# Kernel tuning notes

Measured on AMD Instinct MI355X. Metric: run time of the kernel, lower is better.

Reference implementation:

```python
import jax, jax.numpy as jnp
import numpy as np

B, V, NV, NR, N, E, D, H, OUT, L = 4, 20, 8000, 200, 8000, 200000, 128, 128, 64, 3
DECAY = 0.03


def setup_inputs() -> dict:
    key = jax.random.key(0)
    ks = jax.random.split(key, 16)
    node_ids = jax.random.randint(ks[0], (N,), 0, NV)
    rel_ids = jax.random.randint(ks[1], (E,), 0, NR)
    edge_index = jax.random.randint(ks[2], (2, E), 0, N)
    batch = jnp.repeat(jnp.arange(B), N // B)  # sorted graph assignment, 2000 nodes/graph
    visit_node = (jax.random.uniform(ks[3], (B, V, NV)) < 0.3).astype(jnp.float32)
    ehr_nodes = (jax.random.uniform(ks[4], (B, NV)) < 0.1).astype(jnp.float32)
    s = lambda k, shape: jax.random.normal(k, shape, jnp.float32) * 0.05
    return dict(
        node_ids=node_ids, rel_ids=rel_ids, edge_index=edge_index, batch=batch,
        visit_node=visit_node, ehr_nodes=ehr_nodes,
        node_emb_w=s(ks[5], (NV, D)), rel_emb_w=s(ks[6], (NR, D)),
        lin_w=s(ks[7], (D, H)), lin_b=jnp.zeros((H,), jnp.float32),
        alpha_w=s(ks[8], (L, H)), alpha_b=jnp.zeros((L,), jnp.float32),
        beta_w=s(ks[9], (L, NV)), beta_b=jnp.zeros((L,), jnp.float32),
        conv_w=s(ks[10], (L, H, H)), conv_b=jnp.zeros((L, H), jnp.float32),
        wr_w=s(ks[11], (L, H)), wr_b=jnp.zeros((L,), jnp.float32),
        mlp_w=s(ks[12], (2 * H, OUT)), mlp_b=jnp.zeros((OUT,), jnp.float32),
    )


def reference(node_ids, rel_ids, edge_index, batch, visit_node, ehr_nodes,
              node_emb_w, rel_emb_w, lin_w, lin_b, alpha_w, alpha_b,
              beta_w, beta_b, conv_w, conv_b, wr_w, wr_b, mlp_w, mlp_b):
    # shared input projection (torch: self.lin applied to node and edge embeddings)
    x = node_emb_w[node_ids] @ lin_w + lin_b          # [N,H]
    edge_attr = rel_emb_w[rel_ids] @ lin_w + lin_b    # [E,H]

    # pack per-graph node features into dense [B, NV, H] (x_new in torch, fixed across layers)
    counts = jax.ops.segment_sum(jnp.ones((N,), jnp.float32), batch, B)            # [B]
    starts = jnp.concatenate([jnp.zeros((1,), jnp.int32),
                              jnp.cumsum(counts.astype(jnp.int32))[:-1]])
    local = jnp.arange(N) - starts[batch]                                          # position within graph
    x_pad = jnp.zeros((B, NV, H), jnp.float32).at[batch, local].set(x)

    lam = jnp.exp(DECAY * (V - jnp.arange(V, dtype=jnp.float32)))[None, :, None]   # [1,V,1]
    src, dst = edge_index[0], edge_index[1]
    eb, en = batch[src], node_ids[src]

    for l in range(L):
        # alpha attention over visits (softmax on visit axis)
        feat = visit_node[..., None] * x_pad[:, None]                              # [B,V,NV,H]
        alpha = jax.nn.softmax(jnp.einsum('bvnh,h->bvn', feat, alpha_w[l]) + alpha_b[l], axis=1)
        # beta: time-decayed visit attention
        beta = jnp.tanh(visit_node @ beta_w[l] + beta_b[l])[:, :, None] * lam      # [B,V,1]
        attn_full = alpha * beta                                                   # [B,V,NV]
        attn_e = attn_full[eb, 0, en][:, None]                                     # [E,1] (visit idx 0 as in source)
        # BiAttentionGNNConv: gather-mul-relu-scatter with edge attention
        w_rel = (edge_attr @ wr_w[l] + wr_b[l])[:, None]                           # [E,1]
        msg = jax.nn.relu(x[src] * attn_e + w_rel * edge_attr)                     # [E,H]
        agg = jax.ops.segment_sum(msg, dst, N)                                     # scatter-add to targets
        x = jax.nn.relu((agg + x) @ conv_w[l] + conv_b[l])                         # eps=0 -> (1+eps)*x = x; dropout=eval

    # joint patient representation
    x_graph = jax.ops.segment_sum(x, batch, B) / counts[:, None]                   # global mean pool
    x_node = (ehr_nodes @ node_emb_w) / jnp.sum(ehr_nodes, axis=1, keepdims=True)  # [B,D]
    x_node = x_node @ lin_w + lin_b
    logits = jnp.concatenate([x_graph, x_node], axis=1) @ mlp_w + mlp_b            # [B,OUT]
    return logits
```

## Files before the change

kernel.cpp:

```cpp
#include <hip/hip_runtime.h>

#define NN  8000
#define EE  200000
#define BB  4
#define VV  20
#define NVV 8000
#define NRR 200
#define HH  128
#define OO  64
#define LL  3
#define NPB 8
#define NG  2000

__global__ __launch_bounds__(128) void k_proj_nodes(
    const int* __restrict__ node_ids, const float* __restrict__ emb,
    const float* __restrict__ lin_w, const float* __restrict__ lin_b,
    const float* __restrict__ alpha_w, float* __restrict__ x,
    float* __restrict__ snode)
{
  int blk = blockIdx.x, t = threadIdx.x;
  __shared__ float er[NPB][HH];
  __shared__ float part[LL][NPB][2];
  int base = blk * NPB;
  #pragma unroll
  for (int n = 0; n < NPB; ++n)
    er[n][t] = emb[node_ids[base + n] * HH + t];
  __syncthreads();
  float bt = lin_b[t];
  float acc[NPB];
  #pragma unroll
  for (int n = 0; n < NPB; ++n) acc[n] = bt;
  for (int d4 = 0; d4 < HH / 4; ++d4) {
    float e4[NPB][4];
    #pragma unroll
    for (int n = 0; n < NPB; ++n) {
      float4 v = *(const float4*)&er[n][d4 * 4];
      e4[n][0] = v.x; e4[n][1] = v.y; e4[n][2] = v.z; e4[n][3] = v.w;
    }
    #pragma unroll
    for (int j = 0; j < 4; ++j) {
      float lwv = lin_w[(d4 * 4 + j) * HH + t];
      #pragma unroll
      for (int n = 0; n < NPB; ++n) acc[n] += e4[n][j] * lwv;
    }
  }
  #pragma unroll
  for (int n = 0; n < NPB; ++n) x[(base + n) * HH + t] = acc[n];
  #pragma unroll
  for (int l = 0; l < LL; ++l) {
    float aw = alpha_w[l * HH + t];
    #pragma unroll
    for (int n = 0; n < NPB; ++n) {
      float v = acc[n] * aw;
      for (int off = 32; off > 0; off >>= 1) v += __shfl_down(v, off, 64);
      if ((t & 63) == 0) part[l][n][t >> 6] = v;
    }
  }
  __syncthreads();
  if (t < LL * NPB) {
    int l = t / NPB, n = t % NPB;
    snode[l * NN + base + n] = part[l][n][0] + part[l][n][1];
  }
}

__global__ __launch_bounds__(128) void k_prb(
    const float* __restrict__ rel_emb, const float* __restrict__ lin_w,
    const float* __restrict__ lin_b, const float* __restrict__ wr_w,
    const float* __restrict__ wr_b, const float* __restrict__ visit_node,
    const float* __restrict__ beta_w, const float* __restrict__ beta_b,
    float* __restrict__ wrelp, float* __restrict__ beta0,
    int* __restrict__ iz, float* __restrict__ fz)
{
  int blk = blockIdx.x, t = threadIdx.x;
  int idx = blk * 128 + t;
  if (idx < 2 * NN) iz[idx] = 0;
  if (idx < BB * HH * 2 + BB) fz[idx] = 0.f;
  if (blk < NRR) {
    __shared__ float row[HH];
    __shared__ float part[LL][2];
    row[t] = rel_emb[blk * HH + t];
    __syncthreads();
    float acc = lin_b[t];
    #pragma unroll 4
    for (int d = 0; d < HH; ++d) acc += row[d] * lin_w[d * HH + t];
    #pragma unroll
    for (int l = 0; l < LL; ++l) {
      float v = acc * wr_w[l * HH + t];
      for (int off = 32; off > 0; off >>= 1) v += __shfl_down(v, off, 64);
      if ((t & 63) == 0) part[l][t >> 6] = v;
    }
    __syncthreads();
    #pragma unroll
    for (int l = 0; l < LL; ++l) {
      float rd = part[l][0] + part[l][1] + wr_b[l];
      wrelp[(l * NRR + blk) * HH + t] = rd * acc;
    }
  } else {
    int j = blk - NRR;
    int l = j >> 2, b = j & 3;
    float acc = 0.f;
    for (int n = t; n < NVV; n += 128)
      acc += visit_node[(b * VV + 0) * NVV + n] * beta_w[l * NVV + n];
    for (int off = 32; off > 0; off >>= 1) acc += __shfl_down(acc, off, 64);
    __shared__ float bred[2];
    if ((t & 63) == 0) bred[t >> 6] = acc;
    __syncthreads();
    if (t == 0)
      beta0[l * BB + b] = tanhf(bred[0] + bred[1] + beta_b[l]) * expf(0.03f * 20.0f);
  }
}

__global__ __launch_bounds__(256) void k_anode_hist(
    const int* __restrict__ node_ids, const int* __restrict__ batch,
    const int* __restrict__ edge_index, const float* __restrict__ visit_node,
    const float* __restrict__ snode, const float* __restrict__ alpha_b,
    const float* __restrict__ beta0, float* __restrict__ anode,
    int* __restrict__ deg)
{
  int idx = blockIdx.x * 256 + threadIdx.x;
  if (idx < EE) atomicAdd(&deg[edge_index[EE + idx]], 1);
  if (idx >= NN) return;
  int b = batch[idx], nid = node_ids[idx];
  float vn[VV];
  #pragma unroll
  for (int v = 0; v < VV; ++v) vn[v] = visit_node[(b * VV + v) * NVV + nid];
  #pragma unroll
  for (int l = 0; l < LL; ++l) {
    float s = (nid < NG) ? snode[l * NN + b * NG + nid] : 0.0f;
    float ab = alpha_b[l];
    float m = -1e30f;
    #pragma unroll
    for (int v = 0; v < VV; ++v) m = fmaxf(m, vn[v] * s + ab);
    float sum = 0.f;
    #pragma unroll
    for (int v = 0; v < VV; ++v) sum += expf(vn[v] * s + ab - m);
    anode[l * NN + idx] = (expf(vn[0] * s + ab - m) / sum) * beta0[l * BB + b];
  }
}

__global__ __launch_bounds__(1024) void k_scan(const int* __restrict__ deg,
                                               int* __restrict__ row_ptr)
{
  int t = threadIdx.x;
  __shared__ int ps[1024];
  int local[8];
  int base = t * 8;
  int s = 0;
  #pragma unroll
  for (int j = 0; j < 8; ++j) {
    int idx = base + j;
    int v = (idx < NN) ? deg[idx] : 0;
    local[j] = s; s += v;
  }
  ps[t] = s;
  __syncthreads();
  for (int off = 1; off < 1024; off <<= 1) {
    int v = (t >= off) ? ps[t - off] : 0;
    __syncthreads();
    ps[t] += v;
    __syncthreads();
  }
  int excl = (t == 0) ? 0 : ps[t - 1];
  #pragma unroll
  for (int j = 0; j < 8; ++j) {
    int idx = base + j;
    if (idx < NN) row_ptr[idx] = excl + local[j];
  }
  if (t == 1023) row_ptr[NN] = ps[1023];
}

__global__ void k_scatter(const int* __restrict__ edge_index, const int* __restrict__ rel_ids,
                          const int* __restrict__ row_ptr, int* __restrict__ cursor,
                          int2* __restrict__ csr_sr)
{
  int e = blockIdx.x * 256 + threadIdx.x;
  if (e >= EE) return;
  int dst = edge_index[EE + e];
  int p = row_ptr[dst] + atomicAdd(&cursor[dst], 1);
  csr_sr[p] = make_int2(edge_index[e], rel_ids[e]);
}

__global__ __launch_bounds__(256) void k_gather_conv(
    const int* __restrict__ row_ptr, const int2* __restrict__ csr_sr,
    const float* __restrict__ anode, const float* __restrict__ xin,
    const float* __restrict__ wrelp, const float* __restrict__ conv_w,
    const float* __restrict__ conv_b, float* __restrict__ xout, int l)
{
  int t = threadIdx.x;
  int sub = t >> 5, lane = t & 31;
  int i = blockIdx.x * NPB + sub;
  __shared__ float aggrow[NPB][HH];
  const float4* __restrict__ xin4 = (const float4*)xin;
  const float4* __restrict__ wr4 = (const float4*)wrelp + (size_t)l * NRR * 32;
  const float4* __restrict__ cw4 = (const float4*)conv_w + (size_t)l * HH * 32;
  const float* __restrict__ an = anode + (size_t)l * NN;

  float4 acc = xin4[i * 32 + lane];
  int k0 = row_ptr[i], k1 = row_ptr[i + 1];
  int k = k0;
  for (; k + 3 < k1; k += 4) {
    int2 s0 = csr_sr[k],     s1 = csr_sr[k + 1];
    int2 s2 = csr_sr[k + 2], s3 = csr_sr[k + 3];
    float a0 = an[s0.x], a1 = an[s1.x], a2 = an[s2.x], a3 = an[s3.x];
    float4 x0 = xin4[s0.x * 32 + lane], w0 = wr4[s0.y * 32 + lane];
    float4 x1 = xin4[s1.x * 32 + lane], w1 = wr4[s1.y * 32 + lane];
    float4 x2 = xin4[s2.x * 32 + lane], w2 = wr4[s2.y * 32 + lane];
    float4 x3 = xin4[s3.x * 32 + lane], w3 = wr4[s3.y * 32 + lane];
    acc.x += fmaxf(x0.x * a0 + w0.x, 0.f) + fmaxf(x1.x * a1 + w1.x, 0.f)
           + fmaxf(x2.x * a2 + w2.x, 0.f) + fmaxf(x3.x * a3 + w3.x, 0.f);
    acc.y += fmaxf(x0.y * a0 + w0.y, 0.f) + fmaxf(x1.y * a1 + w1.y, 0.f)
           + fmaxf(x2.y * a2 + w2.y, 0.f) + fmaxf(x3.y * a3 + w3.y, 0.f);
    acc.z += fmaxf(x0.z * a0 + w0.z, 0.f) + fmaxf(x1.z * a1 + w1.z, 0.f)
           + fmaxf(x2.z * a2 + w2.z, 0.f) + fmaxf(x3.z * a3 + w3.z, 0.f);
    acc.w += fmaxf(x0.w * a0 + w0.w, 0.f) + fmaxf(x1.w * a1 + w1.w, 0.f)
           + fmaxf(x2.w * a2 + w2.w, 0.f) + fmaxf(x3.w * a3 + w3.w, 0.f);
  }
  for (; k < k1; ++k) {
    int2 s0 = csr_sr[k];
    float a0 = an[s0.x];
    float4 x0 = xin4[s0.x * 32 + lane], w0 = wr4[s0.y * 32 + lane];
    acc.x += fmaxf(x0.x * a0 + w0.x, 0.f);
    acc.y += fmaxf(x0.y * a0 + w0.y, 0.f);
    acc.z += fmaxf(x0.z * a0 + w0.z, 0.f);
    acc.w += fmaxf(x0.w * a0 + w0.w, 0.f);
  }
  *(float4*)&aggrow[sub][lane * 4] = acc;
  __syncthreads();

  float4 o = ((const float4*)conv_b)[l * 32 + lane];
  for (int d4 = 0; d4 < HH / 4; ++d4) {
    float4 ag = *(const float4*)&aggrow[sub][d4 * 4];
    float4 c0 = cw4[(d4 * 4 + 0) * 32 + lane];
    float4 c1 = cw4[(d4 * 4 + 1) * 32 + lane];
    float4 c2 = cw4[(d4 * 4 + 2) * 32 + lane];
    float4 c3 = cw4[(d4 * 4 + 3) * 32 + lane];
    o.x += ag.x * c0.x + ag.y * c1.x + ag.z * c2.x + ag.w * c3.x;
    o.y += ag.x * c0.y + ag.y * c1.y + ag.z * c2.y + ag.w * c3.y;
    o.z += ag.x * c0.z + ag.y * c1.z + ag.z * c2.z + ag.w * c3.z;
    o.w += ag.x * c0.w + ag.y * c1.w + ag.z * c2.w + ag.w * c3.w;
  }
  o.x = fmaxf(o.x, 0.f); o.y = fmaxf(o.y, 0.f);
  o.z = fmaxf(o.z, 0.f); o.w = fmaxf(o.w, 0.f);
  ((float4*)xout)[i * 32 + lane] = o;
}

__global__ __launch_bounds__(128) void k_pool(
    const float* __restrict__ x, const float* __restrict__ ehr,
    const float* __restrict__ emb, float* __restrict__ xg_raw,
    float* __restrict__ xn_raw, float* __restrict__ denom)
{
  int t = threadIdx.x;
  if (blockIdx.x < 64) {
    int b = blockIdx.x >> 4, c = blockIdx.x & 15;
    const int per = NG / 16;
    int base = b * NG + c * per;
    float acc = 0.f;
    for (int i = 0; i < per; ++i) acc += x[(base + i) * HH + t];
    atomicAdd(&xg_raw[b * HH + t], acc);
  } else {
    int ib = blockIdx.x - 64;
    int b = ib >> 5, c = ib & 31;
    const int per = NVV / 32;
    int base = c * per;
    float acc = 0.f;
    for (int n = base; n < base + per; ++n)
      acc += ehr[b * NVV + n] * emb[n * HH + t];
    atomicAdd(&xn_raw[b * HH + t], acc);
    __shared__ float red[128];
    float dsum = 0.f;
    for (int n = base + t; n < base + per; n += 128) dsum += ehr[b * NVV + n];
    red[t] = dsum;
    __syncthreads();
    for (int s = 64; s > 0; s >>= 1) {
      if (t < s) red[t] += red[t + s];
      __syncthreads();
    }
    if (t == 0) atomicAdd(&denom[b], red[0]);
  }
}

__global__ __launch_bounds__(128) void k_final(
    const float* __restrict__ xg_raw, const float* __restrict__ xn_raw,
    const float* __restrict__ denom, const float* __restrict__ lin_w,
    const float* __restrict__ lin_b, const float* __restrict__ mlp_w,
    const float* __restrict__ mlp_b, float* __restrict__ out)
{
  int b = blockIdx.x, t = threadIdx.x;
  __shared__ float xg[HH], xn[HH], xnp[HH];
  xg[t] = xg_raw[b * HH + t] * (1.0f / NG);
  xn[t] = xn_raw[b * HH + t] / denom[b];
  __syncthreads();
  float a3 = lin_b[t];
  #pragma unroll 4
  for (int d = 0; d < HH; ++d) a3 += xn[d] * lin_w[d * HH + t];
  xnp[t] = a3;
  __syncthreads();
  if (t < OO) {
    float a4 = mlp_b[t];
    #pragma unroll 4
    for (int h = 0; h < HH; ++h)
      a4 += xg[h] * mlp_w[h * OO + t] + xnp[h] * mlp_w[(HH + h) * OO + t];
    out[b * OO + t] = a4;
  }
}

extern "C" void kernel_launch(void* const* d_in, const int* in_sizes, int n_in,
                              void* d_out, int out_size, void* d_ws, size_t ws_size,
                              hipStream_t stream) {
  const int*   node_ids   = (const int*)d_in[0];
  const int*   rel_ids    = (const int*)d_in[1];
  const int*   edge_index = (const int*)d_in[2];
  const int*   batch      = (const int*)d_in[3];
  const float* visit_node = (const float*)d_in[4];
  const float* ehr        = (const float*)d_in[5];
  const float* node_emb   = (const float*)d_in[6];
  const float* rel_emb    = (const float*)d_in[7];
  const float* lin_w      = (const float*)d_in[8];
  const float* lin_b      = (const float*)d_in[9];
  const float* alpha_w    = (const float*)d_in[10];
  const float* alpha_b    = (const float*)d_in[11];
  const float* beta_w     = (const float*)d_in[12];
  const float* beta_b     = (const float*)d_in[13];
  const float* conv_w     = (const float*)d_in[14];
  const float* conv_b     = (const float*)d_in[15];
  const float* wr_w       = (const float*)d_in[16];
  const float* wr_b       = (const float*)d_in[17];
  const float* mlp_w      = (const float*)d_in[18];
  const float* mlp_b      = (const float*)d_in[19];
  float* out = (float*)d_out;

  float* ws = (float*)d_ws;
  float* xA     = ws; ws += NN * HH;
  float* xB     = ws; ws += NN * HH;
  float* wrelp  = ws; ws += LL * NRR * HH;
  float* snode  = ws; ws += LL * NN;
  float* beta0  = ws; ws += LL * BB;
  float* anode  = ws; ws += LL * NN;
  float* xg_raw = ws; ws += BB * HH;
  float* xn_raw = ws; ws += BB * HH;
  float* denom  = ws; ws += BB;
  int* iws      = (int*)ws;
  int* deg      = iws; iws += NN;
  int* cursor   = iws; iws += NN;
  int* row_ptr  = iws; iws += NN + 2;
  int2* csr_sr  = (int2*)iws;

  hipLaunchKernelGGL(k_proj_nodes, dim3(NN / NPB), dim3(HH), 0, stream,
                     node_ids, node_emb, lin_w, lin_b, alpha_w, xA, snode);
  hipLaunchKernelGGL(k_prb, dim3(NRR + LL * BB), dim3(HH), 0, stream,
                     rel_emb, lin_w, lin_b, wr_w, wr_b, visit_node, beta_w,
                     beta_b, wrelp, beta0, deg, xg_raw);
  hipLaunchKernelGGL(k_anode_hist, dim3((EE + 255) / 256), dim3(256), 0, stream,
                     node_ids, batch, edge_index, visit_node, snode, alpha_b,
                     beta0, anode, deg);
  hipLaunchKernelGGL(k_scan, dim3(1), dim3(1024), 0, stream, deg, row_ptr);
  hipLaunchKernelGGL(k_scatter, dim3((EE + 255) / 256), dim3(256), 0, stream,
                     edge_index, rel_ids, row_ptr, cursor, csr_sr);
  const float* xin = xA;
  float* xout = xB;
  for (int l = 0; l < LL; ++l) {
    hipLaunchKernelGGL(k_gather_conv, dim3(NN / NPB), dim3(256), 0, stream,
                       row_ptr, csr_sr, anode, xin, wrelp, conv_w, conv_b, xout, l);
    const float* tmp = xin; xin = xout; xout = (float*)tmp;
  }
  hipLaunchKernelGGL(k_pool, dim3(64 + 128), dim3(HH), 0, stream,
                     xB, ehr, node_emb, xg_raw, xn_raw, denom);
  hipLaunchKernelGGL(k_final, dim3(BB), dim3(HH), 0, stream,
                     xg_raw, xn_raw, denom, lin_w, lin_b, mlp_w, mlp_b, out);
}
```

Measured before the change: 311.3 us.

## Split each node's edge gather across two half-warps and halve nodes per block

Each node's incoming-edge list is now split between two 32-lane groups, and the partial sums are combined through shared memory. This halves the serial gather chain per node and doubles the number of blocks to raise memory-level parallelism. The dense conv matmul is redistributed so 64 lanes each produce a float2 of output. In exchange it adds extra shared-memory traffic and synchronisation, and the conv-weight loads are now amortised over 4 nodes per block instead of 8.

```diff
diff --git a/kernel.cpp b/kernel.cpp
--- a/kernel.cpp
+++ b/kernel.cpp
@@ -10,6 +10,7 @@
 #define OO  64
 #define LL  3
 #define NPB 8
+#define NPG 4
 #define NG  2000
 
 __global__ __launch_bounds__(128) void k_proj_nodes(
@@ -187,18 +188,27 @@
     const float* __restrict__ conv_b, float* __restrict__ xout, int l)
 {
   int t = threadIdx.x;
-  int sub = t >> 5, lane = t & 31;
-  int i = blockIdx.x * NPB + sub;
-  __shared__ float aggrow[NPB][HH];
+  int node_sub = t >> 6;
+  int half = (t >> 5) & 1;
+  int lane = t & 31;
+  int lane64 = t & 63;
+  int i = blockIdx.x * NPG + node_sub;
+  __shared__ float part[2][NPG][HH];
   const float4* __restrict__ xin4 = (const float4*)xin;
+  const float2* __restrict__ xin2 = (const float2*)xin;
   const float4* __restrict__ wr4 = (const float4*)wrelp + (size_t)l * NRR * 32;
-  const float4* __restrict__ cw4 = (const float4*)conv_w + (size_t)l * HH * 32;
   const float* __restrict__ an = anode + (size_t)l * NN;
 
-  float4 acc = xin4[i * 32 + lane];
   int k0 = row_ptr[i], k1 = row_ptr[i + 1];
-  int k = k0;
-  for (; k + 3 < k1; k += 4) {
+  int cnt = k1 - k0;
+  int halfcnt = (cnt + 1) >> 1;
+  int ks = k0 + half * halfcnt;
+  int ke = half ? k1 : (k0 + halfcnt);
+
+  float4 accA = make_float4(0.f, 0.f, 0.f, 0.f);
+  float4 accB = make_float4(0.f, 0.f, 0.f, 0.f);
+  int k = ks;
+  for (; k + 3 < ke; k += 4) {
     int2 s0 = csr_sr[k],     s1 = csr_sr[k + 1];
     int2 s2 = csr_sr[k + 2], s3 = csr_sr[k + 3];
     float a0 = an[s0.x], a1 = an[s1.x], a2 = an[s2.x], a3 = an[s3.x];
@@ -206,42 +216,52 @@
     float4 x1 = xin4[s1.x * 32 + lane], w1 = wr4[s1.y * 32 + lane];
     float4 x2 = xin4[s2.x * 32 + lane], w2 = wr4[s2.y * 32 + lane];
     float4 x3 = xin4[s3.x * 32 + lane], w3 = wr4[s3.y * 32 + lane];
-    acc.x += fmaxf(x0.x * a0 + w0.x, 0.f) + fmaxf(x1.x * a1 + w1.x, 0.f)
-           + fmaxf(x2.x * a2 + w2.x, 0.f) + fmaxf(x3.x * a3 + w3.x, 0.f);
-    acc.y += fmaxf(x0.y * a0 + w0.y, 0.f) + fmaxf(x1.y * a1 + w1.y, 0.f)
-           + fmaxf(x2.y * a2 + w2.y, 0.f) + fmaxf(x3.y * a3 + w3.y, 0.f);
-    acc.z += fmaxf(x0.z * a0 + w0.z, 0.f) + fmaxf(x1.z * a1 + w1.z, 0.f)
-           + fmaxf(x2.z * a2 + w2.z, 0.f) + fmaxf(x3.z * a3 + w3.z, 0.f);
-    acc.w += fmaxf(x0.w * a0 + w0.w, 0.f) + fmaxf(x1.w * a1 + w1.w, 0.f)
-           + fmaxf(x2.w * a2 + w2.w, 0.f) + fmaxf(x3.w * a3 + w3.w, 0.f);
-  }
-  for (; k < k1; ++k) {
+    accA.x += fmaxf(x0.x * a0 + w0.x, 0.f) + fmaxf(x1.x * a1 + w1.x, 0.f);
+    accA.y += fmaxf(x0.y * a0 + w0.y, 0.f) + fmaxf(x1.y * a1 + w1.y, 0.f);
+    accA.z += fmaxf(x0.z * a0 + w0.z, 0.f) + fmaxf(x1.z * a1 + w1.z, 0.f);
+    accA.w += fmaxf(x0.w * a0 + w0.w, 0.f) + fmaxf(x1.w * a1 + w1.w, 0.f);
+    accB.x += fmaxf(x2.x * a2 + w2.x, 0.f) + fmaxf(x3.x * a3 + w3.x, 0.f);
+    accB.y += fmaxf(x2.y * a2 + w2.y, 0.f) + fmaxf(x3.y * a3 + w3.y, 0.f);
+    accB.z += fmaxf(x2.z * a2 + w2.z, 0.f) + fmaxf(x3.z * a3 + w3.z, 0.f);
+    accB.w += fmaxf(x2.w * a2 + w2.w, 0.f) + fmaxf(x3.w * a3 + w3.w, 0.f);
+  }
+  for (; k < ke; ++k) {
     int2 s0 = csr_sr[k];
     float a0 = an[s0.x];
     float4 x0 = xin4[s0.x * 32 + lane], w0 = wr4[s0.y * 32 + lane];
-    acc.x += fmaxf(x0.x * a0 + w0.x, 0.f);
-    acc.y += fmaxf(x0.y * a0 + w0.y, 0.f);
-    acc.z += fmaxf(x0.z * a0 + w0.z, 0.f);
-    acc.w += fmaxf(x0.w * a0 + w0.w, 0.f);
-  }
-  *(float4*)&aggrow[sub][lane * 4] = acc;
-  __syncthreads();
-
-  float4 o = ((const float4*)conv_b)[l * 32 + lane];
+    accA.x += fmaxf(x0.x * a0 + w0.x, 0.f);
+    accA.y += fmaxf(x0.y * a0 + w0.y, 0.f);
+    accA.z += fmaxf(x0.z * a0 + w0.z, 0.f);
+    accA.w += fmaxf(x0.w * a0 + w0.w, 0.f);
+  }
+  accA.x += accB.x; accA.y += accB.y; accA.z += accB.z; accA.w += accB.w;
+  *(float4*)&part[half][node_sub][lane * 4] = accA;
+  __syncthreads();
+
+  {
+    float2 p0 = *(const float2*)&part[0][node_sub][lane64 * 2];
+    float2 p1 = *(const float2*)&part[1][node_sub][lane64 * 2];
+    float2 xi = xin2[(size_t)i * 64 + lane64];
+    float2 ag = make_float2(xi.x + p0.x + p1.x, xi.y + p0.y + p1.y);
+    __syncthreads();
+    *(float2*)&part[0][node_sub][lane64 * 2] = ag;
+  }
+  __syncthreads();
+
+  const float2* __restrict__ cwb = (const float2*)conv_w + (size_t)l * HH * 64;
+  float2 o = ((const float2*)conv_b)[l * 64 + lane64];
   for (int d4 = 0; d4 < HH / 4; ++d4) {
-    float4 ag = *(const float4*)&aggrow[sub][d4 * 4];
-    float4 c0 = cw4[(d4 * 4 + 0) * 32 + lane];
-    float4 c1 = cw4[(d4 * 4 + 1) * 32 + lane];
-    float4 c2 = cw4[(d4 * 4 + 2) * 32 + lane];
-    float4 c3 = cw4[(d4 * 4 + 3) * 32 + lane];
-    o.x += ag.x * c0.x + ag.y * c1.x + ag.z * c2.x + ag.w * c3.x;
-    o.y += ag.x * c0.y + ag.y * c1.y + ag.z * c2.y + ag.w * c3.y;
-    o.z += ag.x * c0.z + ag.y * c1.z + ag.z * c2.z + ag.w * c3.z;
-    o.w += ag.x * c0.w + ag.y * c1.w + ag.z * c2.w + ag.w * c3.w;
-  }
-  o.x = fmaxf(o.x, 0.f); o.y = fmaxf(o.y, 0.f);
-  o.z = fmaxf(o.z, 0.f); o.w = fmaxf(o.w, 0.f);
-  ((float4*)xout)[i * 32 + lane] = o;
+    float4 agv = *(const float4*)&part[0][node_sub][d4 * 4];
+    float2 c0 = cwb[(d4 * 4 + 0) * 64 + lane64];
+    float2 c1 = cwb[(d4 * 4 + 1) * 64 + lane64];
+    float2 c2 = cwb[(d4 * 4 + 2) * 64 + lane64];
+    float2 c3 = cwb[(d4 * 4 + 3) * 64 + lane64];
+    o.x += agv.x * c0.x + agv.y * c1.x + agv.z * c2.x + agv.w * c3.x;
+    o.y += agv.x * c0.y + agv.y * c1.y + agv.z * c2.y + agv.w * c3.y;
+  }
+  o.x = fmaxf(o.x, 0.f);
+  o.y = fmaxf(o.y, 0.f);
+  ((float2*)xout)[(size_t)i * 64 + lane64] = o;
 }
 
 __global__ __launch_bounds__(128) void k_pool(
@@ -359,7 +379,7 @@
   const float* xin = xA;
   float* xout = xB;
   for (int l = 0; l < LL; ++l) {
-    hipLaunchKernelGGL(k_gather_conv, dim3(NN / NPB), dim3(256), 0, stream,
+    hipLaunchKernelGGL(k_gather_conv, dim3(NN / NPG), dim3(256), 0, stream,
                        row_ptr, csr_sr, anode, xin, wrelp, conv_w, conv_b, xout, l);
     const float* tmp = xin; xin = xout; xout = (float*)tmp;
   }
```

Result: slower. 352.5 us (+13.2%).
